# Optimization experiments

Measured on AMD Instinct MI355X. Metric: run time of the kernel, lower is better.

Reference implementation:

```python
import jax, jax.numpy as jnp
import numpy as np

# Model dims
B, S, H = 1, 1024, 2048
NH, NKV, DH = 32, 8, 64
G = NH // NKV            # GQA group size
E, K, I = 8, 2, 2048     # experts, top_k, intermediate
ALPHA, LIMIT = 1.702, 7.0
EPS = 1e-5
SCALE = DH ** -0.5


def rmsnorm(x, g):
    return x * jax.lax.rsqrt(jnp.mean(x * x, axis=-1, keepdims=True) + EPS) * g


def setup_inputs() -> dict:
    key = jax.random.key(0)
    ks = jax.random.split(key, 24)
    w = lambda k, shp: jax.random.normal(k, shp, dtype=jnp.float32) * 0.02
    causal = jnp.where(jnp.tril(jnp.ones((S, S), dtype=bool)), 0.0, -1e9).astype(jnp.float32)
    return {
        "hidden_states": jax.random.normal(ks[0], (B, S, H), dtype=jnp.float32),
        "attention_bias": causal[None, None, :, :],           # [1,1,S,S]
        "ln1_g": jnp.ones((H,), jnp.float32),
        "ln2_g": jnp.ones((H,), jnp.float32),
        "Wq": w(ks[1], (NH * DH, H)),  "bq": w(ks[2], (NH * DH,)),
        "Wk": w(ks[3], (NKV * DH, H)), "bk": w(ks[4], (NKV * DH,)),
        "Wv": w(ks[5], (NKV * DH, H)), "bv": w(ks[6], (NKV * DH,)),
        "Wo": w(ks[7], (H, NH * DH)),  "bo": w(ks[8], (H,)),
        "sinks": w(ks[9], (NH,)),
        "router_w": w(ks[10], (E, H)), "router_b": w(ks[11], (E,)),
        "We_gate": w(ks[12], (E, I, H)), "be_gate": w(ks[13], (E, I)),
        "We_up":   w(ks[14], (E, I, H)), "be_up":   w(ks[15], (E, I)),
        "We_down": w(ks[16], (E, H, I)), "be_down": w(ks[17], (E, H)),
    }


def reference(hidden_states, attention_bias, ln1_g, ln2_g,
              Wq, bq, Wk, bk, Wv, bv, Wo, bo, sinks,
              router_w, router_b,
              We_gate, be_gate, We_up, be_up, We_down, be_down):
    x = hidden_states
    # ---- pre-norm sink attention ----
    xn = rmsnorm(x, ln1_g)
    q = (xn @ Wq.T + bq).reshape(B, S, NH, DH).transpose(0, 2, 1, 3)    # [B,NH,S,DH]
    k = (xn @ Wk.T + bk).reshape(B, S, NKV, DH).transpose(0, 2, 1, 3)   # [B,NKV,S,DH]
    v = (xn @ Wv.T + bv).reshape(B, S, NKV, DH).transpose(0, 2, 1, 3)
    # GQA: replicate each kv head G times consecutively (repeat_kv)
    k = jnp.repeat(k, G, axis=1)
    v = jnp.repeat(v, G, axis=1)
    scores = jnp.einsum('bhqd,bhkd->bhqk', q, k) * SCALE + attention_bias  # [B,NH,S,S]
    sink_col = jnp.broadcast_to(sinks.reshape(1, NH, 1, 1), (B, NH, S, 1))
    combined = jnp.concatenate([scores, sink_col], axis=-1)               # [B,NH,S,S+1]
    probs = jax.nn.softmax(combined, axis=-1)[..., :-1]                   # drop sink
    attn = jnp.einsum('bhqk,bhkd->bhqd', probs, v)
    attn = attn.transpose(0, 2, 1, 3).reshape(B, S, NH * DH)
    h = x + (attn @ Wo.T + bo)
    # ---- pre-norm MoE FFN ----
    hn = rmsnorm(h, ln2_g)
    router_logits = hn @ router_w.T + router_b                            # [B,S,E]
    rw, sel = jax.lax.top_k(router_logits, K)
    rw = jax.nn.softmax(rw, axis=-1)                                      # [B,S,K]
    # dense per-expert MLP over all tokens (matches the exported loop)
    gate = jnp.einsum('bsh,eih->bsei', hn, We_gate) + be_gate             # [B,S,E,I]
    up = jnp.einsum('bsh,eih->bsei', hn, We_up) + be_up
    gate_c = jnp.minimum(gate, LIMIT)
    up_c = jnp.clip(up, -LIMIT, LIMIT)
    glu = gate_c * jax.nn.sigmoid(ALPHA * gate_c)
    gated = (up_c + 1.0) * glu
    down = jnp.einsum('bsei,ehi->bseh', gated, We_down) + be_down         # [B,S,E,H]
    # per-token expert weight: sum_k rw * (sel == e)
    wts = jnp.sum(rw[..., None] * (sel[..., None] == jnp.arange(E)), axis=2)  # [B,S,E]
    moe = jnp.einsum('bseh,bse->bsh', down, wts)
    return h + moe
```

## Files before the change

kernel.cpp:

```cpp
#include <hip/hip_runtime.h>
#include <hip/hip_bf16.h>

#define HD 2048
#define SEQ 1024
#define NHEAD 32
#define NKVH 8
#define DHEAD 64
#define NEXP 8
#define INTER 2048
#define SCALE 0.125f
#define ALPHA 1.702f
#define LIMIT 7.0f

typedef __attribute__((ext_vector_type(8))) short short8;
typedef __attribute__((ext_vector_type(4))) short short4v;
typedef __attribute__((ext_vector_type(4))) float f32x4;

__device__ __forceinline__ unsigned short f2bf(float f) {
  union { float f; unsigned u; } v; v.f = f;
  unsigned r = v.u + 0x7fffu + ((v.u >> 16) & 1u);
  return (unsigned short)(r >> 16);
}
__device__ __forceinline__ float bf2f(unsigned short h) {
  union { unsigned u; float f; } v; v.u = ((unsigned)h) << 16; return v.f;
}
__device__ __forceinline__ void split2(float f, unsigned short& hi, unsigned short& lo) {
  hi = f2bf(f);
  lo = f2bf(f - bf2f(hi));
}

__device__ __forceinline__ f32x4 mfma32(short8 a, short8 b, f32x4 c) {
  return __builtin_amdgcn_mfma_f32_16x16x32_bf16(a, b, c, 0, 0, 0);
}

__device__ __forceinline__ void gl_lds16(const float* g, float* l) {
  __builtin_amdgcn_global_load_lds(
      (const __attribute__((address_space(1))) unsigned int*)g,
      (__attribute__((address_space(3))) unsigned int*)l, 16, 0, 0);
}

__global__ __launch_bounds__(256) void rmsnorm_split_kernel(
    const float* __restrict__ x, const float* __restrict__ gamma,
    unsigned short* __restrict__ oh, unsigned short* __restrict__ ol) {
  int row = blockIdx.x, tid = threadIdx.x;
  const float* xr = x + (size_t)row * HD;
  float v[8];
#pragma unroll
  for (int i = 0; i < 8; ++i) v[i] = xr[tid * 8 + i];
  float ss = 0.f;
#pragma unroll
  for (int i = 0; i < 8; ++i) ss += v[i] * v[i];
#pragma unroll
  for (int off = 32; off; off >>= 1) ss += __shfl_xor(ss, off, 64);
  __shared__ float wss[4];
  if ((tid & 63) == 0) wss[tid >> 6] = ss;
  __syncthreads();
  float rs = rsqrtf((wss[0] + wss[1] + wss[2] + wss[3]) * (1.0f / HD) + 1e-5f);
  short8 vh, vl;
#pragma unroll
  for (int i = 0; i < 8; ++i) {
    float val = v[i] * rs * gamma[tid * 8 + i];
    unsigned short h, lo;
    split2(val, h, lo);
    vh[i] = (short)h;
    vl[i] = (short)lo;
  }
  *(short8*)(oh + (size_t)row * HD + tid * 8) = vh;
  *(short8*)(ol + (size_t)row * HD + tid * 8) = vl;
}

__global__ __launch_bounds__(256) void rmsnorm_plain_kernel(
    const float* __restrict__ x, const float* __restrict__ gamma,
    unsigned short* __restrict__ out) {
  int row = blockIdx.x, tid = threadIdx.x;
  const float* xr = x + (size_t)row * HD;
  float v[8];
#pragma unroll
  for (int i = 0; i < 8; ++i) v[i] = xr[tid * 8 + i];
  float ss = 0.f;
#pragma unroll
  for (int i = 0; i < 8; ++i) ss += v[i] * v[i];
#pragma unroll
  for (int off = 32; off; off >>= 1) ss += __shfl_xor(ss, off, 64);
  __shared__ float wss[4];
  if ((tid & 63) == 0) wss[tid >> 6] = ss;
  __syncthreads();
  float rs = rsqrtf((wss[0] + wss[1] + wss[2] + wss[3]) * (1.0f / HD) + 1e-5f);
  short8 o;
#pragma unroll
  for (int i = 0; i < 8; ++i) o[i] = (short)f2bf(v[i] * rs * gamma[tid * 8 + i]);
  *(short8*)(out + (size_t)row * HD + tid * 8) = o;
}

template <int MT, int NS, bool SPLIT, int EPI>
__global__ __launch_bounds__(256) void gemm_gl(
    const unsigned short* __restrict__ Ah, const unsigned short* __restrict__ Al,
    int ldA,
    const float* __restrict__ W0, const float* __restrict__ W1,
    const float* __restrict__ W2,
    const float* __restrict__ b0, const float* __restrict__ b1,
    const float* __restrict__ b2,
    const float* __restrict__ resid,
    const int* __restrict__ counts, const int* __restrict__ arows,
    const int* __restrict__ orows,
    unsigned short* __restrict__ oh0, unsigned short* __restrict__ ol0,
    unsigned short* __restrict__ oh1, unsigned short* __restrict__ ol1,
    unsigned short* __restrict__ oh2, unsigned short* __restrict__ ol2,
    float* __restrict__ f0, float* __restrict__ f1,
    int M, int Kd) {
  constexpr int MG = MT * 64;
  constexpr int NR = NS * 16;
  constexpr int RPW = NR / 4;
  constexpr int NI = RPW / 4;
  __shared__ __align__(16) float lw[2][NR][64];
  int tid = threadIdx.x, l = tid & 63, w = tid >> 6;
  int g = l >> 4, q = l & 15;
  int n0 = blockIdx.x * NR;

  const float* Wb;
  const float* bias;
  int nloc = n0, e = 0, mat = 0;
  if constexpr (EPI == 0) {
    if (n0 < NHEAD * DHEAD) {
      Wb = W0; bias = b0;
    } else if (n0 < NHEAD * DHEAD + NKVH * DHEAD) {
      Wb = W1; bias = b1; nloc = n0 - NHEAD * DHEAD;
    } else {
      Wb = W2; bias = b2; nloc = n0 - (NHEAD * DHEAD + NKVH * DHEAD);
    }
  } else if constexpr (EPI == 1) {
    Wb = W0; bias = b0;
  } else if constexpr (EPI == 2) {
    e = blockIdx.z >> 1;
    mat = blockIdx.z & 1;
    Wb = (mat ? W1 : W0) + (size_t)e * INTER * HD;
    bias = (mat ? b1 : b0) + (size_t)e * INTER;
  } else {
    e = blockIdx.z;
    Wb = W0 + (size_t)e * HD * INTER;
    bias = b0 + (size_t)e * HD;
  }
  int cnt = (EPI >= 2) ? counts[e] : M;

  const float* sptr[NI];
  float* sdst0[NI];
  float* sdst1[NI];
#pragma unroll
  for (int j = 0; j < NI; ++j) {
    int r = RPW * w + 4 * j + (l >> 4);
    int gs = ((l & 15) ^ (r & 7)) * 4;
    sptr[j] = Wb + (size_t)(nloc + r) * Kd + gs;
    sdst0[j] = &lw[0][RPW * w + 4 * j][0];
    sdst1[j] = &lw[1][RPW * w + 4 * j][0];
  }
  auto stage = [&](int buf, int kc) {
#pragma unroll
    for (int j = 0; j < NI; ++j)
      gl_lds16(sptr[j] + kc, buf ? sdst1[j] : sdst0[j]);
  };

  int mstart = (EPI <= 1) ? blockIdx.y : 0;
  int mstep = (EPI <= 1) ? gridDim.y : 1;

  for (int mg = mstart; mg * MG < cnt; mg += mstep) {
    int mb = mg * MG + w * (MT * 16);
    const unsigned short* ap[MT];
    const unsigned short* apl[MT];
#pragma unroll
    for (int mt = 0; mt < MT; ++mt) {
      int mm = min(mb + mt * 16 + q, cnt - 1);
      int ar = (EPI >= 2) ? arows[e * SEQ + mm] : mm;
      ap[mt] = Ah + (size_t)ar * ldA + 8 * g;
      if constexpr (SPLIT) apl[mt] = Al + (size_t)ar * ldA + 8 * g;
    }
    f32x4 acc[MT][NS];
#pragma unroll
    for (int mt = 0; mt < MT; ++mt)
#pragma unroll
      for (int ns = 0; ns < NS; ++ns) acc[mt][ns] = (f32x4){0.f, 0.f, 0.f, 0.f};

    stage(0, 0);
    short8 ab[2][MT], abl[2][MT];
#pragma unroll
    for (int mt = 0; mt < MT; ++mt) {
      ab[0][mt] = *(const short8*)(ap[mt]);
      ab[1][mt] = *(const short8*)(ap[mt] + 32);
      if constexpr (SPLIT) {
        abl[0][mt] = *(const short8*)(apl[mt]);
        abl[1][mt] = *(const short8*)(apl[mt] + 32);
      }
    }
    __syncthreads();

    int nc = Kd / 64;
    for (int c = 0; c < nc; ++c) {
      int u = c & 1;
      if (c + 1 < nc) stage(u ^ 1, (c + 1) * 64);
#pragma unroll
      for (int kh = 0; kh < 2; ++kh) {
        short8 acur[MT], acl[MT];
#pragma unroll
        for (int mt = 0; mt < MT; ++mt) {
          acur[mt] = ab[kh][mt];
          if constexpr (SPLIT) acl[mt] = abl[kh][mt];
        }
        int kn = c * 64 + kh * 32 + 64;
        if (kn < Kd) {
#pragma unroll
          for (int mt = 0; mt < MT; ++mt) {
            ab[kh][mt] = *(const short8*)(ap[mt] + kn);
            if constexpr (SPLIT) abl[kh][mt] = *(const short8*)(apl[mt] + kn);
          }
        }
        short8 wh[NS], wl[NS];
#pragma unroll
        for (int ns = 0; ns < NS; ++ns) {
          int row = ns * 16 + q;
          int r7 = q & 7;
          int i0 = ((kh * 8 + g * 2) ^ r7) * 16;
          int i1 = ((kh * 8 + g * 2 + 1) ^ r7) * 16;
          const char* base = (const char*)&lw[u][row][0];
          float4 v0 = *(const float4*)(base + i0);
          float4 v1 = *(const float4*)(base + i1);
          float vv[8] = {v0.x, v0.y, v0.z, v0.w, v1.x, v1.y, v1.z, v1.w};
#pragma unroll
          for (int jj = 0; jj < 8; ++jj) {
            if constexpr (SPLIT) {
              unsigned short h, lo;
              split2(vv[jj], h, lo);
              wh[ns][jj] = (short)h;
              wl[ns][jj] = (short)lo;
            } else {
              wh[ns][jj] = (short)f2bf(vv[jj]);
            }
          }
        }
#pragma unroll
        for (int mt = 0; mt < MT; ++mt)
#pragma unroll
          for (int ns = 0; ns < NS; ++ns) {
            acc[mt][ns] = mfma32(acur[mt], wh[ns], acc[mt][ns]);
            if constexpr (SPLIT) {
              acc[mt][ns] = mfma32(acur[mt], wl[ns], acc[mt][ns]);
              acc[mt][ns] = mfma32(acl[mt], wh[ns], acc[mt][ns]);
            }
          }
      }
      __syncthreads();
    }
#pragma unroll
    for (int ns = 0; ns < NS; ++ns) {
      int ncol = nloc + ns * 16 + q;
      float bs = bias[ncol];
#pragma unroll
      for (int mt = 0; mt < MT; ++mt) {
#pragma unroll
        for (int r = 0; r < 4; ++r) {
          int mr = mb + mt * 16 + 4 * g + r;
          float val = acc[mt][ns][r] + bs;
          if constexpr (EPI == 0) {
            unsigned short h, lo;
            split2(val, h, lo);
            if (n0 < NHEAD * DHEAD) {
              oh0[(size_t)mr * (NHEAD * DHEAD) + ncol] = h;
              ol0[(size_t)mr * (NHEAD * DHEAD) + ncol] = lo;
            } else if (n0 < NHEAD * DHEAD + NKVH * DHEAD) {
              oh1[(size_t)mr * (NKVH * DHEAD) + ncol] = h;
              ol1[(size_t)mr * (NKVH * DHEAD) + ncol] = lo;
            } else {
              oh2[(size_t)ncol * SEQ + mr] = h;
              ol2[(size_t)ncol * SEQ + mr] = lo;
            }
          } else if constexpr (EPI == 1) {
            f0[(size_t)mr * HD + ncol] = val + resid[(size_t)mr * HD + ncol];
          } else if constexpr (EPI == 2) {
            if (mr < cnt) {
              int slot = orows[e * SEQ + mr];
              (mat ? f1 : f0)[(size_t)slot * INTER + ncol] = val;
            }
          } else {
            if (mr < cnt) {
              int slot = orows[e * SEQ + mr];
              f0[(size_t)slot * HD + ncol] = val;
            }
          }
        }
      }
    }
  }
}

__global__ __launch_bounds__(256) void attn_kernel(
    const unsigned short* __restrict__ Qh, const unsigned short* __restrict__ Ql,
    const unsigned short* __restrict__ Kh, const unsigned short* __restrict__ Kl,
    const unsigned short* __restrict__ Vh, const unsigned short* __restrict__ Vl,
    const float* __restrict__ sinks, unsigned short* __restrict__ outh,
    unsigned short* __restrict__ outl) {
  __shared__ __align__(16) unsigned short pbuf[4][2][16][40];
  int l = threadIdx.x & 63, widx = threadIdx.x >> 6;
  int wid = blockIdx.x * 4 + widx;
  int head = wid >> 6, qt = wid & 63;
  int q0 = qt * 16;
  int g = l >> 4, q = l & 15;
  int kvh = head >> 2;
  size_t qoff = (size_t)(q0 + q) * (NHEAD * DHEAD) + head * DHEAD + 8 * g;
  short8 qh0 = *(const short8*)(Qh + qoff);
  short8 qh1 = *(const short8*)(Qh + qoff + 32);
  short8 ql0 = *(const short8*)(Ql + qoff);
  short8 ql1 = *(const short8*)(Ql + qoff + 32);
  float m = sinks[head];
  float lsum = 1.0f;
  f32x4 o[4] = {{0, 0, 0, 0}, {0, 0, 0, 0}, {0, 0, 0, 0}, {0, 0, 0, 0}};
  int qglob = q0 + q;
  for (int kt = 0; kt <= qt; kt += 2) {
    bool hasB = (kt + 1) <= qt;
    size_t koff = (size_t)(kt * 16 + q) * (NKVH * DHEAD) + kvh * DHEAD + 8 * g;
    f32x4 stA = {0, 0, 0, 0};
    {
      short8 kh0 = *(const short8*)(Kh + koff);
      short8 kh1 = *(const short8*)(Kh + koff + 32);
      short8 kl0 = *(const short8*)(Kl + koff);
      short8 kl1 = *(const short8*)(Kl + koff + 32);
      stA = mfma32(kh0, qh0, stA);
      stA = mfma32(kh0, ql0, stA);
      stA = mfma32(kl0, qh0, stA);
      stA = mfma32(kh1, qh1, stA);
      stA = mfma32(kh1, ql1, stA);
      stA = mfma32(kl1, qh1, stA);
    }
    f32x4 stB = {0, 0, 0, 0};
    if (hasB) {
      size_t koff2 = koff + (size_t)16 * (NKVH * DHEAD);
      short8 kh0 = *(const short8*)(Kh + koff2);
      short8 kh1 = *(const short8*)(Kh + koff2 + 32);
      short8 kl0 = *(const short8*)(Kl + koff2);
      short8 kl1 = *(const short8*)(Kl + koff2 + 32);
      stB = mfma32(kh0, qh0, stB);
      stB = mfma32(kh0, ql0, stB);
      stB = mfma32(kl0, qh0, stB);
      stB = mfma32(kh1, qh1, stB);
      stB = mfma32(kh1, ql1, stB);
      stB = mfma32(kl1, qh1, stB);
    }
    float sA[4], sB[4];
#pragma unroll
    for (int r = 0; r < 4; ++r) {
      int keyA = kt * 16 + 4 * g + r;
      sA[r] = (keyA <= qglob) ? stA[r] * SCALE : -1e30f;
      sB[r] = (hasB && keyA + 16 <= qglob) ? stB[r] * SCALE : -1e30f;
    }
    float mt = fmaxf(fmaxf(fmaxf(sA[0], sA[1]), fmaxf(sA[2], sA[3])),
                     fmaxf(fmaxf(sB[0], sB[1]), fmaxf(sB[2], sB[3])));
    mt = fmaxf(mt, __shfl_xor(mt, 16, 64));
    mt = fmaxf(mt, __shfl_xor(mt, 32, 64));
    float mnew = fmaxf(m, mt);
    float corr = __expf(m - mnew);
    float pA[4], pB[4];
    float rsum = 0.f;
#pragma unroll
    for (int r = 0; r < 4; ++r) {
      pA[r] = __expf(sA[r] - mnew);
      pB[r] = __expf(sB[r] - mnew);
      rsum += pA[r] + pB[r];
    }
    rsum += __shfl_xor(rsum, 16, 64);
    rsum += __shfl_xor(rsum, 32, 64);
    lsum = lsum * corr + rsum;
    m = mnew;
#pragma unroll
    for (int dt = 0; dt < 4; ++dt)
#pragma unroll
      for (int r = 0; r < 4; ++r) o[dt][r] *= corr;
    unsigned short ph[8], pl[8];
#pragma unroll
    for (int r = 0; r < 4; ++r) {
      split2(pA[r], ph[r], pl[r]);
      split2(pB[r], ph[4 + r], pl[4 + r]);
    }
    short4v wAh = {(short)ph[0], (short)ph[1], (short)ph[2], (short)ph[3]};
    short4v wBh = {(short)ph[4], (short)ph[5], (short)ph[6], (short)ph[7]};
    short4v wAl = {(short)pl[0], (short)pl[1], (short)pl[2], (short)pl[3]};
    short4v wBl = {(short)pl[4], (short)pl[5], (short)pl[6], (short)pl[7]};
    *(short4v*)&pbuf[widx][0][q][4 * g] = wAh;
    *(short4v*)&pbuf[widx][0][q][16 + 4 * g] = wBh;
    *(short4v*)&pbuf[widx][1][q][4 * g] = wAl;
    *(short4v*)&pbuf[widx][1][q][16 + 4 * g] = wBl;
    asm volatile("s_waitcnt lgkmcnt(0)" ::: "memory");
    short8 pbh = *(const short8*)&pbuf[widx][0][q][8 * g];
    short8 pbl = *(const short8*)&pbuf[widx][1][q][8 * g];
    size_t vbase = (size_t)(kvh * DHEAD) * SEQ + kt * 16 + 8 * g;
#pragma unroll
    for (int dt = 0; dt < 4; ++dt) {
      size_t voff = vbase + (size_t)(dt * 16 + q) * SEQ;
      short8 vh8 = *(const short8*)(Vh + voff);
      short8 vl8 = *(const short8*)(Vl + voff);
      o[dt] = mfma32(vh8, pbh, o[dt]);
      o[dt] = mfma32(vh8, pbl, o[dt]);
      o[dt] = mfma32(vl8, pbh, o[dt]);
    }
  }
  float inv = 1.0f / lsum;
#pragma unroll
  for (int dt = 0; dt < 4; ++dt)
#pragma unroll
    for (int r = 0; r < 4; ++r) {
      float val = o[dt][r] * inv;
      unsigned short h, lo;
      split2(val, h, lo);
      size_t idx = (size_t)qglob * (NHEAD * DHEAD) + head * DHEAD + dt * 16 + 4 * g + r;
      outh[idx] = h;
      outl[idx] = lo;
    }
}

__global__ __launch_bounds__(64) void router_kernel(
    const float* __restrict__ h, const float* __restrict__ gamma,
    const float* __restrict__ rw, const float* __restrict__ rb,
    float* __restrict__ wsel, int* __restrict__ counts,
    int* __restrict__ lists, int* __restrict__ slotof) {
  int t = blockIdx.x;
  int l = threadIdx.x;
  const float* hr = h + (size_t)t * HD;
  double ss = 0.0;
  for (int i = l; i < HD; i += 64) {
    double x = (double)hr[i];
    ss += x * x;
  }
#pragma unroll
  for (int off = 32; off; off >>= 1) ss += __shfl_xor(ss, off, 64);
  double rs = rsqrt(ss * (1.0 / HD) + 1e-5);
  double acc[NEXP];
#pragma unroll
  for (int e = 0; e < NEXP; ++e) acc[e] = 0.0;
  for (int i = l; i < HD; i += 64) {
    double xh = (double)hr[i] * rs * (double)gamma[i];
#pragma unroll
    for (int e = 0; e < NEXP; ++e) acc[e] += xh * (double)rw[e * HD + i];
  }
#pragma unroll
  for (int e = 0; e < NEXP; ++e)
#pragma unroll
    for (int off = 32; off; off >>= 1) acc[e] += __shfl_xor(acc[e], off, 64);
  if (l == 0) {
    double lg[NEXP];
#pragma unroll
    for (int e = 0; e < NEXP; ++e) lg[e] = acc[e] + (double)rb[e];
    int e0 = 0;
#pragma unroll
    for (int e = 1; e < NEXP; ++e)
      if (lg[e] > lg[e0]) e0 = e;
    int e1 = -1;
#pragma unroll
    for (int e = 0; e < NEXP; ++e)
      if (e != e0 && (e1 < 0 || lg[e] > lg[e1])) e1 = e;
    double d = exp(lg[e1] - lg[e0]);
    float p0 = (float)(1.0 / (1.0 + d)), p1 = (float)(d / (1.0 + d));
    wsel[2 * t] = p0;
    wsel[2 * t + 1] = p1;
    int s0 = atomicAdd(&counts[e0], 1);
    lists[e0 * SEQ + s0] = t;
    slotof[e0 * SEQ + s0] = 2 * t;
    int s1 = atomicAdd(&counts[e1], 1);
    lists[e1 * SEQ + s1] = t;
    slotof[e1 * SEQ + s1] = 2 * t + 1;
  }
}

__global__ __launch_bounds__(256) void act_kernel(
    const float* __restrict__ rg, const float* __restrict__ ru,
    unsigned short* __restrict__ gated) {
  size_t base = (size_t)blockIdx.x * INTER + threadIdx.x * 8;
  float4 g0 = *(const float4*)(rg + base);
  float4 g1 = *(const float4*)(rg + base + 4);
  float4 u0 = *(const float4*)(ru + base);
  float4 u1 = *(const float4*)(ru + base + 4);
  float gv[8] = {g0.x, g0.y, g0.z, g0.w, g1.x, g1.y, g1.z, g1.w};
  float uv[8] = {u0.x, u0.y, u0.z, u0.w, u1.x, u1.y, u1.z, u1.w};
  short8 o;
#pragma unroll
  for (int j = 0; j < 8; ++j) {
    float gc = fminf(gv[j], LIMIT);
    float uc = fminf(fmaxf(uv[j], -LIMIT), LIMIT);
    float glu = gc / (1.f + __expf(-ALPHA * gc));
    o[j] = (short)f2bf((uc + 1.f) * glu);
  }
  *(short8*)(gated + base) = o;
}

__global__ __launch_bounds__(256) void reduce_kernel(
    const float* __restrict__ hbuf, const float* __restrict__ scr,
    const float* __restrict__ wsel, float* __restrict__ out) {
  int t = blockIdx.x;
  int c = threadIdx.x * 8;
  float w0 = wsel[2 * t], w1 = wsel[2 * t + 1];
  size_t hb = (size_t)t * HD + c;
  size_t s0 = (size_t)(2 * t) * HD + c;
  size_t s1 = (size_t)(2 * t + 1) * HD + c;
#pragma unroll
  for (int j = 0; j < 2; ++j) {
    float4 hv = *(const float4*)(hbuf + hb + 4 * j);
    float4 a = *(const float4*)(scr + s0 + 4 * j);
    float4 b = *(const float4*)(scr + s1 + 4 * j);
    float4 r;
    r.x = hv.x + w0 * a.x + w1 * b.x;
    r.y = hv.y + w0 * a.y + w1 * b.y;
    r.z = hv.z + w0 * a.z + w1 * b.z;
    r.w = hv.w + w0 * a.w + w1 * b.w;
    *(float4*)(out + hb + 4 * j) = r;
  }
}

extern "C" void kernel_launch(void* const* d_in, const int* in_sizes, int n_in,
                              void* d_out, int out_size, void* d_ws,
                              size_t ws_size, hipStream_t stream) {
  const float* x = (const float*)d_in[0];
  const float* ln1 = (const float*)d_in[2];
  const float* ln2 = (const float*)d_in[3];
  const float* Wq = (const float*)d_in[4];
  const float* bq = (const float*)d_in[5];
  const float* Wk = (const float*)d_in[6];
  const float* bk = (const float*)d_in[7];
  const float* Wv = (const float*)d_in[8];
  const float* bv = (const float*)d_in[9];
  const float* Wo = (const float*)d_in[10];
  const float* bo = (const float*)d_in[11];
  const float* sinks = (const float*)d_in[12];
  const float* rw = (const float*)d_in[13];
  const float* rb = (const float*)d_in[14];
  const float* Wg = (const float*)d_in[15];
  const float* bg = (const float*)d_in[16];
  const float* Wu = (const float*)d_in[17];
  const float* bu = (const float*)d_in[18];
  const float* Wd = (const float*)d_in[19];
  const float* bd = (const float*)d_in[20];
  float* out = (float*)d_out;

  char* ws = (char*)d_ws;
  size_t off = 0;
  auto alloc = [&](size_t bytes) {
    void* p = ws + off;
    off += (bytes + 255) & ~(size_t)255;
    return p;
  };
  unsigned short* xnh = (unsigned short*)alloc((size_t)SEQ * HD * 2);
  unsigned short* xnl = (unsigned short*)alloc((size_t)SEQ * HD * 2);
  unsigned short* qbh = (unsigned short*)alloc((size_t)SEQ * NHEAD * DHEAD * 2);
  unsigned short* qbl = (unsigned short*)alloc((size_t)SEQ * NHEAD * DHEAD * 2);
  unsigned short* kbh = (unsigned short*)alloc((size_t)SEQ * NKVH * DHEAD * 2);
  unsigned short* kbl = (unsigned short*)alloc((size_t)SEQ * NKVH * DHEAD * 2);
  unsigned short* vth = (unsigned short*)alloc((size_t)NKVH * DHEAD * SEQ * 2);
  unsigned short* vtl = (unsigned short*)alloc((size_t)NKVH * DHEAD * SEQ * 2);
  unsigned short* ath = (unsigned short*)alloc((size_t)SEQ * NHEAD * DHEAD * 2);
  unsigned short* atl = (unsigned short*)alloc((size_t)SEQ * NHEAD * DHEAD * 2);
  float* hbuf = (float*)alloc((size_t)SEQ * HD * 4);
  unsigned short* hn = (unsigned short*)alloc((size_t)SEQ * HD * 2);
  float* wsel = (float*)alloc((size_t)SEQ * 2 * 4);
  int* counts = (int*)alloc(NEXP * 4);
  int* lists = (int*)alloc((size_t)NEXP * SEQ * 4);
  int* slotof = (int*)alloc((size_t)NEXP * SEQ * 4);
  float* rawg = (float*)alloc((size_t)2 * SEQ * INTER * 4);
  float* rawu = (float*)alloc((size_t)2 * SEQ * INTER * 4);
  unsigned short* gated = (unsigned short*)alloc((size_t)2 * SEQ * INTER * 2);
  float* scr = rawg;
  (void)ws_size;
  (void)off;

  rmsnorm_split_kernel<<<SEQ, 256, 0, stream>>>(x, ln1, xnh, xnl);
  gemm_gl<4, 2, true, 0><<<dim3(96, 4, 1), 256, 0, stream>>>(
      xnh, xnl, HD, Wq, Wk, Wv, bq, bk, bv, nullptr, nullptr, nullptr, nullptr,
      qbh, qbl, kbh, kbl, vth, vtl, nullptr, nullptr, SEQ, HD);
  attn_kernel<<<NHEAD * 64 / 4, 256, 0, stream>>>(qbh, qbl, kbh, kbl, vth, vtl,
                                                  sinks, ath, atl);
  gemm_gl<4, 2, true, 1><<<dim3(64, 4, 1), 256, 0, stream>>>(
      ath, atl, NHEAD * DHEAD, Wo, nullptr, nullptr, bo, nullptr, nullptr, x,
      nullptr, nullptr, nullptr, nullptr, nullptr, nullptr, nullptr, nullptr,
      nullptr, hbuf, nullptr, SEQ, NHEAD * DHEAD);
  rmsnorm_plain_kernel<<<SEQ, 256, 0, stream>>>(hbuf, ln2, hn);
  hipMemsetAsync(counts, 0, NEXP * sizeof(int), stream);
  router_kernel<<<SEQ, 64, 0, stream>>>(hbuf, ln2, rw, rb, wsel, counts, lists,
                                        slotof);
  gemm_gl<5, 4, false, 2><<<dim3(32, 1, 16), 256, 0, stream>>>(
      hn, nullptr, HD, Wg, Wu, nullptr, bg, bu, nullptr, nullptr, counts, lists,
      slotof, nullptr, nullptr, nullptr, nullptr, nullptr, nullptr, rawg, rawu,
      SEQ, HD);
  act_kernel<<<2 * SEQ, 256, 0, stream>>>(rawg, rawu, gated);
  gemm_gl<5, 2, false, 3><<<dim3(64, 1, 8), 256, 0, stream>>>(
      gated, nullptr, INTER, Wd, nullptr, nullptr, bd, nullptr, nullptr,
      nullptr, counts, slotof, slotof, nullptr, nullptr, nullptr, nullptr,
      nullptr, nullptr, scr, nullptr, SEQ, INTER);
  reduce_kernel<<<SEQ, 256, 0, stream>>>(hbuf, scr, wsel, out);
}
```

Baseline: 606.6 us.

## Fuse gate/up expert GEMMs with the SwiGLU activation epilogue

Computes the gate and up projections for an expert in the same block by staging both weight tiles into LDS and keeping two accumulator sets. The clamped GLU activation is applied in the epilogue, which writes bf16 gated values directly. This removes the separate activation kernel and the fp32 round trip of raw gate/up outputs through global memory. The cost is a larger LDS footprint and more accumulator registers per block, which may lower occupancy. The grid changes from 16 z-slices with NS=4 to 8 z-slices with NS=2.

```diff
diff --git a/kernel.cpp b/kernel.cpp
--- a/kernel.cpp
+++ b/kernel.cpp
@@ -106,52 +106,56 @@
     unsigned short* __restrict__ oh0, unsigned short* __restrict__ ol0,
     unsigned short* __restrict__ oh1, unsigned short* __restrict__ ol1,
     unsigned short* __restrict__ oh2, unsigned short* __restrict__ ol2,
-    float* __restrict__ f0, float* __restrict__ f1,
+    float* __restrict__ f0, unsigned short* __restrict__ gated,
     int M, int Kd) {
-  constexpr int MG = MT * 64;
   constexpr int NR = NS * 16;
-  constexpr int RPW = NR / 4;
-  constexpr int NI = RPW / 4;
-  __shared__ __align__(16) float lw[2][NR][64];
+  constexpr int NMAT = (EPI == 4) ? 2 : 1;
+  constexpr int NI = NMAT * NR / 16;
+  __shared__ __align__(16) float lw[2][NMAT][NR][64];
   int tid = threadIdx.x, l = tid & 63, w = tid >> 6;
   int g = l >> 4, q = l & 15;
   int n0 = blockIdx.x * NR;
 
-  const float* Wb;
+  const float* WbM[NMAT];
   const float* bias;
-  int nloc = n0, e = 0, mat = 0;
+  const float* bias2 = nullptr;
+  int nloc = n0, e = 0;
   if constexpr (EPI == 0) {
     if (n0 < NHEAD * DHEAD) {
-      Wb = W0; bias = b0;
+      WbM[0] = W0; bias = b0;
     } else if (n0 < NHEAD * DHEAD + NKVH * DHEAD) {
-      Wb = W1; bias = b1; nloc = n0 - NHEAD * DHEAD;
+      WbM[0] = W1; bias = b1; nloc = n0 - NHEAD * DHEAD;
     } else {
-      Wb = W2; bias = b2; nloc = n0 - (NHEAD * DHEAD + NKVH * DHEAD);
+      WbM[0] = W2; bias = b2; nloc = n0 - (NHEAD * DHEAD + NKVH * DHEAD);
     }
   } else if constexpr (EPI == 1) {
-    Wb = W0; bias = b0;
-  } else if constexpr (EPI == 2) {
-    e = blockIdx.z >> 1;
-    mat = blockIdx.z & 1;
-    Wb = (mat ? W1 : W0) + (size_t)e * INTER * HD;
-    bias = (mat ? b1 : b0) + (size_t)e * INTER;
+    WbM[0] = W0; bias = b0;
+  } else if constexpr (EPI == 3) {
+    e = blockIdx.z;
+    WbM[0] = W0 + (size_t)e * HD * INTER;
+    bias = b0 + (size_t)e * HD;
   } else {
     e = blockIdx.z;
-    Wb = W0 + (size_t)e * HD * INTER;
-    bias = b0 + (size_t)e * HD;
-  }
-  int cnt = (EPI >= 2) ? counts[e] : M;
+    WbM[0] = W0 + (size_t)e * INTER * HD;
+    WbM[1] = W1 + (size_t)e * INTER * HD;
+    bias = b0 + (size_t)e * INTER;
+    bias2 = b1 + (size_t)e * INTER;
+  }
+  int cnt = (EPI >= 3) ? counts[e] : M;
 
   const float* sptr[NI];
   float* sdst0[NI];
   float* sdst1[NI];
 #pragma unroll
   for (int j = 0; j < NI; ++j) {
-    int r = RPW * w + 4 * j + (l >> 4);
+    int gi = w * NI + j;
+    int mat = gi / (NR / 4);
+    int rr = (gi % (NR / 4)) * 4;
+    int r = rr + (l >> 4);
     int gs = ((l & 15) ^ (r & 7)) * 4;
-    sptr[j] = Wb + (size_t)(nloc + r) * Kd + gs;
-    sdst0[j] = &lw[0][RPW * w + 4 * j][0];
-    sdst1[j] = &lw[1][RPW * w + 4 * j][0];
+    sptr[j] = WbM[mat] + (size_t)(nloc + r) * Kd + gs;
+    sdst0[j] = &lw[0][mat][rr][0];
+    sdst1[j] = &lw[1][mat][rr][0];
   }
   auto stage = [&](int buf, int kc) {
 #pragma unroll
@@ -161,6 +165,7 @@
 
   int mstart = (EPI <= 1) ? blockIdx.y : 0;
   int mstep = (EPI <= 1) ? gridDim.y : 1;
+  constexpr int MG = MT * 64;
 
   for (int mg = mstart; mg * MG < cnt; mg += mstep) {
     int mb = mg * MG + w * (MT * 16);
@@ -169,15 +174,18 @@
 #pragma unroll
     for (int mt = 0; mt < MT; ++mt) {
       int mm = min(mb + mt * 16 + q, cnt - 1);
-      int ar = (EPI >= 2) ? arows[e * SEQ + mm] : mm;
+      int ar = (EPI >= 3) ? arows[e * SEQ + mm] : mm;
       ap[mt] = Ah + (size_t)ar * ldA + 8 * g;
       if constexpr (SPLIT) apl[mt] = Al + (size_t)ar * ldA + 8 * g;
     }
-    f32x4 acc[MT][NS];
-#pragma unroll
-    for (int mt = 0; mt < MT; ++mt)
-#pragma unroll
-      for (int ns = 0; ns < NS; ++ns) acc[mt][ns] = (f32x4){0.f, 0.f, 0.f, 0.f};
+    f32x4 acc[NMAT][MT][NS];
+#pragma unroll
+    for (int m2 = 0; m2 < NMAT; ++m2)
+#pragma unroll
+      for (int mt = 0; mt < MT; ++mt)
+#pragma unroll
+        for (int ns = 0; ns < NS; ++ns)
+          acc[m2][mt][ns] = (f32x4){0.f, 0.f, 0.f, 0.f};
 
     stage(0, 0);
     short8 ab[2][MT], abl[2][MT];
@@ -212,39 +220,43 @@
             if constexpr (SPLIT) abl[kh][mt] = *(const short8*)(apl[mt] + kn);
           }
         }
-        short8 wh[NS], wl[NS];
-#pragma unroll
-        for (int ns = 0; ns < NS; ++ns) {
-          int row = ns * 16 + q;
-          int r7 = q & 7;
-          int i0 = ((kh * 8 + g * 2) ^ r7) * 16;
-          int i1 = ((kh * 8 + g * 2 + 1) ^ r7) * 16;
-          const char* base = (const char*)&lw[u][row][0];
-          float4 v0 = *(const float4*)(base + i0);
-          float4 v1 = *(const float4*)(base + i1);
-          float vv[8] = {v0.x, v0.y, v0.z, v0.w, v1.x, v1.y, v1.z, v1.w};
-#pragma unroll
-          for (int jj = 0; jj < 8; ++jj) {
-            if constexpr (SPLIT) {
-              unsigned short h, lo;
-              split2(vv[jj], h, lo);
-              wh[ns][jj] = (short)h;
-              wl[ns][jj] = (short)lo;
-            } else {
-              wh[ns][jj] = (short)f2bf(vv[jj]);
+        short8 wh[NMAT][NS], wl[NMAT][NS];
+#pragma unroll
+        for (int m2 = 0; m2 < NMAT; ++m2)
+#pragma unroll
+          for (int ns = 0; ns < NS; ++ns) {
+            int row = ns * 16 + q;
+            int r7 = q & 7;
+            int i0 = ((kh * 8 + g * 2) ^ r7) * 16;
+            int i1 = ((kh * 8 + g * 2 + 1) ^ r7) * 16;
+            const char* base = (const char*)&lw[u][m2][row][0];
+            float4 v0 = *(const float4*)(base + i0);
+            float4 v1 = *(const float4*)(base + i1);
+            float vv[8] = {v0.x, v0.y, v0.z, v0.w, v1.x, v1.y, v1.z, v1.w};
+#pragma unroll
+            for (int jj = 0; jj < 8; ++jj) {
+              if constexpr (SPLIT) {
+                unsigned short h, lo;
+                split2(vv[jj], h, lo);
+                wh[m2][ns][jj] = (short)h;
+                wl[m2][ns][jj] = (short)lo;
+              } else {
+                wh[m2][ns][jj] = (short)f2bf(vv[jj]);
+              }
             }
           }
-        }
-#pragma unroll
-        for (int mt = 0; mt < MT; ++mt)
-#pragma unroll
-          for (int ns = 0; ns < NS; ++ns) {
-            acc[mt][ns] = mfma32(acur[mt], wh[ns], acc[mt][ns]);
-            if constexpr (SPLIT) {
-              acc[mt][ns] = mfma32(acur[mt], wl[ns], acc[mt][ns]);
-              acc[mt][ns] = mfma32(acl[mt], wh[ns], acc[mt][ns]);
+#pragma unroll
+        for (int m2 = 0; m2 < NMAT; ++m2)
+#pragma unroll
+          for (int mt = 0; mt < MT; ++mt)
+#pragma unroll
+            for (int ns = 0; ns < NS; ++ns) {
+              acc[m2][mt][ns] = mfma32(acur[mt], wh[m2][ns], acc[m2][mt][ns]);
+              if constexpr (SPLIT) {
+                acc[m2][mt][ns] = mfma32(acur[mt], wl[m2][ns], acc[m2][mt][ns]);
+                acc[m2][mt][ns] = mfma32(acl[mt], wh[m2][ns], acc[m2][mt][ns]);
+              }
             }
-          }
       }
       __syncthreads();
     }
@@ -252,12 +264,13 @@
     for (int ns = 0; ns < NS; ++ns) {
       int ncol = nloc + ns * 16 + q;
       float bs = bias[ncol];
+      float bs2 = (EPI == 4) ? bias2[ncol] : 0.f;
 #pragma unroll
       for (int mt = 0; mt < MT; ++mt) {
 #pragma unroll
         for (int r = 0; r < 4; ++r) {
           int mr = mb + mt * 16 + 4 * g + r;
-          float val = acc[mt][ns][r] + bs;
+          float val = acc[0][mt][ns][r] + bs;
           if constexpr (EPI == 0) {
             unsigned short h, lo;
             split2(val, h, lo);
@@ -273,15 +286,19 @@
             }
           } else if constexpr (EPI == 1) {
             f0[(size_t)mr * HD + ncol] = val + resid[(size_t)mr * HD + ncol];
-          } else if constexpr (EPI == 2) {
+          } else if constexpr (EPI == 3) {
             if (mr < cnt) {
               int slot = orows[e * SEQ + mr];
-              (mat ? f1 : f0)[(size_t)slot * INTER + ncol] = val;
+              f0[(size_t)slot * HD + ncol] = val;
             }
           } else {
             if (mr < cnt) {
               int slot = orows[e * SEQ + mr];
-              f0[(size_t)slot * HD + ncol] = val;
+              float up = acc[1][mt][ns][r] + bs2;
+              float gc = fminf(val, LIMIT);
+              float uc = fminf(fmaxf(up, -LIMIT), LIMIT);
+              float glu = gc / (1.f + __expf(-ALPHA * gc));
+              gated[(size_t)slot * INTER + ncol] = f2bf((uc + 1.f) * glu);
             }
           }
         }
@@ -466,27 +483,6 @@
   }
 }
 
-__global__ __launch_bounds__(256) void act_kernel(
-    const float* __restrict__ rg, const float* __restrict__ ru,
-    unsigned short* __restrict__ gated) {
-  size_t base = (size_t)blockIdx.x * INTER + threadIdx.x * 8;
-  float4 g0 = *(const float4*)(rg + base);
-  float4 g1 = *(const float4*)(rg + base + 4);
-  float4 u0 = *(const float4*)(ru + base);
-  float4 u1 = *(const float4*)(ru + base + 4);
-  float gv[8] = {g0.x, g0.y, g0.z, g0.w, g1.x, g1.y, g1.z, g1.w};
-  float uv[8] = {u0.x, u0.y, u0.z, u0.w, u1.x, u1.y, u1.z, u1.w};
-  short8 o;
-#pragma unroll
-  for (int j = 0; j < 8; ++j) {
-    float gc = fminf(gv[j], LIMIT);
-    float uc = fminf(fmaxf(uv[j], -LIMIT), LIMIT);
-    float glu = gc / (1.f + __expf(-ALPHA * gc));
-    o[j] = (short)f2bf((uc + 1.f) * glu);
-  }
-  *(short8*)(gated + base) = o;
-}
-
 __global__ __launch_bounds__(256) void reduce_kernel(
     const float* __restrict__ hbuf, const float* __restrict__ scr,
     const float* __restrict__ wsel, float* __restrict__ out) {
@@ -558,10 +554,8 @@
   int* counts = (int*)alloc(NEXP * 4);
   int* lists = (int*)alloc((size_t)NEXP * SEQ * 4);
   int* slotof = (int*)alloc((size_t)NEXP * SEQ * 4);
-  float* rawg = (float*)alloc((size_t)2 * SEQ * INTER * 4);
-  float* rawu = (float*)alloc((size_t)2 * SEQ * INTER * 4);
   unsigned short* gated = (unsigned short*)alloc((size_t)2 * SEQ * INTER * 2);
-  float* scr = rawg;
+  float* scr = (float*)alloc((size_t)2 * SEQ * HD * 4);
   (void)ws_size;
   (void)off;
 
@@ -579,11 +573,10 @@
   hipMemsetAsync(counts, 0, NEXP * sizeof(int), stream);
   router_kernel<<<SEQ, 64, 0, stream>>>(hbuf, ln2, rw, rb, wsel, counts, lists,
                                         slotof);
-  gemm_gl<5, 4, false, 2><<<dim3(32, 1, 16), 256, 0, stream>>>(
+  gemm_gl<5, 2, false, 4><<<dim3(64, 1, 8), 256, 0, stream>>>(
       hn, nullptr, HD, Wg, Wu, nullptr, bg, bu, nullptr, nullptr, counts, lists,
-      slotof, nullptr, nullptr, nullptr, nullptr, nullptr, nullptr, rawg, rawu,
-      SEQ, HD);
-  act_kernel<<<2 * SEQ, 256, 0, stream>>>(rawg, rawu, gated);
+      slotof, nullptr, nullptr, nullptr, nullptr, nullptr, nullptr, nullptr,
+      gated, SEQ, HD);
   gemm_gl<5, 2, false, 3><<<dim3(64, 1, 8), 256, 0, stream>>>(
       gated, nullptr, INTER, Wd, nullptr, nullptr, bd, nullptr, nullptr,
       nullptr, counts, slotof, slotof, nullptr, nullptr, nullptr, nullptr,
```

After: 596.4 us. About the same (-1.7%).
